# Kernel optimization log

Hardware: AMD Instinct MI355X
Metric: run time of the kernel (lower is better)

Reference implementation:

```python
import jax, jax.numpy as jnp
import numpy as np

N = 8192
C_IN = 512
C_INTER = 128  # in_channels // unit_nums = 512 // 4


def setup_inputs() -> dict:
    key = jax.random.key(0)
    ks = jax.random.split(key, 6)
    x = jax.random.normal(ks[0], (N, C_IN), dtype=jnp.float32)
    # Linear weights init: normal(0, 0.01); biases zero. Stored as [in, out].
    Wg = 0.01 * jax.random.normal(ks[1], (C_IN, C_INTER), dtype=jnp.float32)
    Wt = 0.01 * jax.random.normal(ks[2], (C_IN, C_INTER), dtype=jnp.float32)
    Wp = 0.01 * jax.random.normal(ks[3], (C_IN, C_INTER), dtype=jnp.float32)
    bg = jnp.zeros((C_INTER,), dtype=jnp.float32)
    bt = jnp.zeros((C_INTER,), dtype=jnp.float32)
    bp = jnp.zeros((C_INTER,), dtype=jnp.float32)
    # 1x1 conv weight (1, 2*C_INTER, 1, 1) flattened: first half hits theta, second half phi
    wcat = 0.01 * jax.random.normal(ks[4], (2 * C_INTER,), dtype=jnp.float32)
    return {"x": x, "Wg": Wg, "bg": bg, "Wt": Wt, "bt": bt, "Wp": Wp, "bp": bp, "wcat": wcat}


def reference(x, Wg, bg, Wt, bt, Wp, bp, wcat):
    n = x.shape[0]
    g_x = x @ Wg + bg          # [N, C_inter]
    theta = x @ Wt + bt        # [N, C_inter]
    phi = x @ Wp + bp          # [N, C_inter]
    c = theta.shape[1]
    # 1x1 conv over cat([theta_i, phi_j]) == w1.theta_i + w2.phi_j (outer sum), then ReLU
    a = theta @ wcat[:c]       # [N]
    b = phi @ wcat[c:]         # [N]
    f = jax.nn.relu(a[:, None] + b[None, :])  # [N, N]
    z = (f / n) @ g_x          # [N, C_inter]
    return z
```

## Files before the change

kernel.cpp:

```cpp
#include <hip/hip_runtime.h>

#define C_IN   512
#define C_INT  128
#define NBUCK  1024
#define NMAX   8192

typedef _Float16 half8 __attribute__((ext_vector_type(8)));
typedef short short8 __attribute__((ext_vector_type(8)));
typedef float floatx4 __attribute__((ext_vector_type(4)));


__device__ __forceinline__ int bucket_of(float v, float bmin, float inv_w) {
    float fk = (v - bmin) * inv_w;
    fk = fminf(fmaxf(fk, 0.f), (float)(NBUCK - 1));
    return (int)fk;
}

__device__ __forceinline__ short bf16rnd(float v) {
    unsigned u = __float_as_uint(v);
    return (short)((u + 0x7fffu + ((u >> 16) & 1u)) >> 16);
}


__global__ __launch_bounds__(256) void prep_kernel(
        const float* __restrict__ Wt, const float* __restrict__ Wp,
        const float* __restrict__ Wg, const float* __restrict__ wcat,
        const float* __restrict__ bt, const float* __restrict__ bp,
        float* __restrict__ ut, float* __restrict__ up, float* __restrict__ scal,
        unsigned short* __restrict__ WgT) {
    int t = threadIdx.x, bk = blockIdx.x;
    if (bk < 16) {
        const float* W  = (bk < 8) ? Wt : Wp;
        const float* wv = wcat + ((bk < 8) ? 0 : C_INT);
        float* dst      = (bk < 8) ? ut : up;
        int k = (bk & 7) * 64 + (t >> 2);
        int q = t & 3;
        const float4* row = (const float4*)(W + (size_t)k * C_INT);
        const float4* cv4 = (const float4*)wv;
        float s = 0.f;
        #pragma unroll
        for (int i = 0; i < 8; ++i) {
            float4 a = row[q * 8 + i];
            float4 c = cv4[q * 8 + i];
            s += a.x * c.x + a.y * c.y + a.z * c.z + a.w * c.w;
        }
        s += __shfl_xor(s, 1);
        s += __shfl_xor(s, 2);
        if (q == 0) dst[k] = s;
    } else if (bk == 16) {
        float sumsq = 0.f;
        const float4* w2v = (const float4*)(wcat + C_INT);
        for (int r = 0; r < 2; ++r) {
            int k = t * 2 + r;
            const float4* row = (const float4*)(Wp + (size_t)k * C_INT);
            float d = 0.f;
            #pragma unroll
            for (int i = 0; i < 32; ++i) {
                float4 a4 = row[i]; float4 c4 = w2v[i];
                d += a4.x * c4.x + a4.y * c4.y + a4.z * c4.z + a4.w * c4.w;
            }
            sumsq += d * d;
        }
        float s1p = (t < C_INT) ? bt[t] * wcat[t] : 0.f;
        float s2p = (t < C_INT) ? bp[t] * wcat[C_INT + t] : 0.f;
        for (int off = 32; off; off >>= 1) {
            s1p   += __shfl_down(s1p, off);
            s2p   += __shfl_down(s2p, off);
            sumsq += __shfl_down(sumsq, off);
        }
        __shared__ float red[12];
        int w = t >> 6, lane = t & 63;
        if (lane == 0) { red[w] = s1p; red[4 + w] = s2p; red[8 + w] = sumsq; }
        __syncthreads();
        if (t == 0) {
            float s0 = red[0] + red[1] + red[2] + red[3];
            float s1 = red[4] + red[5] + red[6] + red[7];
            float sq = red[8] + red[9] + red[10] + red[11];
            float sigma = sqrtf(sq);
            scal[0] = s0; scal[1] = s1;
            if (sigma > 1e-20f) {
                scal[2] = s1 - 8.f * sigma;
                scal[3] = (float)NBUCK / (16.f * sigma);
            } else {
                scal[2] = s1 - 1.f; scal[3] = 0.f;
            }
        }
    } else {
        __shared__ float tile[64][132];
        int kb = (bk - 17) * 64;
        #pragma unroll
        for (int it = 0; it < 8; ++it) {
            int idx = it * 256 + t;
            int r = idx >> 5, c4 = idx & 31;
            *(float4*)&tile[r][c4 * 4] =
                ((const float4*)(Wg + (size_t)(kb + r) * C_INT))[c4];
        }
        __syncthreads();
        int n = t & 127, kc = (t >> 7) * 32;
        unsigned pk[16];
        #pragma unroll
        for (int i = 0; i < 16; ++i) {
            unsigned lo = (unsigned short)bf16rnd(tile[kc + 2 * i][n]);
            unsigned hi = (unsigned short)bf16rnd(tile[kc + 2 * i + 1][n]);
            pk[i] = lo | (hi << 16);
        }
        uint4* dst = (uint4*)(WgT + (size_t)n * C_IN + kb + kc);
        #pragma unroll
        for (int i2 = 0; i2 < 4; ++i2) dst[i2] = *(uint4*)&pk[i2 * 4];
    }
}


__global__ __launch_bounds__(64) void gemm_mfma(
        const float* __restrict__ x, const unsigned short* __restrict__ WgT,
        const float* __restrict__ bg,
        const float* __restrict__ ut, const float* __restrict__ up,
        const float* __restrict__ scal,
        _Float16* __restrict__ g, float* __restrict__ a, float* __restrict__ b) {
    int lane = threadIdx.x;
    int i0 = blockIdx.x * 16;
    int m = lane & 15, q = lane >> 4;
    floatx4 accg[8] = {};
    floatx4 accab = {};
    const float* xrow = x + (size_t)(i0 + m) * C_IN + q * 8;
    const float* absrc = (m == 0) ? ut : up;
    #pragma unroll
    for (int ks = 0; ks < 16; ++ks) {
        int k0 = ks * 32;
        float4 f0 = *(const float4*)(xrow + k0);
        float4 f1 = *(const float4*)(xrow + k0 + 4);
        short8 af;
        af[0] = bf16rnd(f0.x); af[1] = bf16rnd(f0.y);
        af[2] = bf16rnd(f0.z); af[3] = bf16rnd(f0.w);
        af[4] = bf16rnd(f1.x); af[5] = bf16rnd(f1.y);
        af[6] = bf16rnd(f1.z); af[7] = bf16rnd(f1.w);
        short8 abf = {};
        if (m < 2) {
            float4 u0 = *(const float4*)(absrc + k0 + q * 8);
            float4 u1 = *(const float4*)(absrc + k0 + q * 8 + 4);
            abf[0] = bf16rnd(u0.x); abf[1] = bf16rnd(u0.y);
            abf[2] = bf16rnd(u0.z); abf[3] = bf16rnd(u0.w);
            abf[4] = bf16rnd(u1.x); abf[5] = bf16rnd(u1.y);
            abf[6] = bf16rnd(u1.z); abf[7] = bf16rnd(u1.w);
        }
        accab = __builtin_amdgcn_mfma_f32_16x16x32_bf16(af, abf, accab, 0, 0, 0);
        #pragma unroll
        for (int f = 0; f < 8; ++f) {
            short8 bfr = *(const short8*)(WgT + (size_t)(f * 16 + m) * C_IN + k0 + q * 8);
            accg[f] = __builtin_amdgcn_mfma_f32_16x16x32_bf16(af, bfr, accg[f], 0, 0, 0);
        }
    }
    #pragma unroll
    for (int f = 0; f < 8; ++f) {
        int col = f * 16 + m;
        float bgv = bg[col];
        #pragma unroll
        for (int r = 0; r < 4; ++r) {
            int row = i0 + q * 4 + r;
            g[(size_t)row * C_INT + col] = (_Float16)(accg[f][r] + bgv);
        }
    }
    if (m < 2) {
        float off = m ? scal[1] : scal[0];
        float* dst = m ? b : a;
        #pragma unroll
        for (int r = 0; r < 4; ++r) dst[i0 + q * 4 + r] = accab[r] + off;
    }
}


__global__ __launch_bounds__(1024) void bucketsuffix_kernel(
        const _Float16* __restrict__ g, const float* __restrict__ b,
        const float* __restrict__ scal,
        unsigned* __restrict__ offs_g, unsigned* __restrict__ list_g,
        float* __restrict__ P1, float* __restrict__ P2, int n) {
    __shared__ float bl[NMAX];
    __shared__ unsigned short ls[NMAX];
    __shared__ unsigned oh[NBUCK];
    __shared__ unsigned cur[NBUCK];
    __shared__ unsigned wtu[16];
    __shared__ float wt1[16], wt2[16];
    int t = threadIdx.x, c = blockIdx.x;
    int lane = t & 63, wv = t >> 6;
    float bmin = scal[2], inv_w = scal[3];
    ((float4*)bl)[t]        = ((const float4*)b)[t];
    ((float4*)bl)[1024 + t] = ((const float4*)b)[1024 + t];
    oh[t] = 0u; cur[t] = 0u;
    __syncthreads();
    int kb_[8];
    #pragma unroll
    for (int r = 0; r < 8; ++r) {
        kb_[r] = bucket_of(bl[t * 8 + r], bmin, inv_w);
        atomicAdd(&oh[kb_[r]], 1u);
    }
    __syncthreads();
    unsigned v = oh[t];
    #pragma unroll
    for (int d = 1; d < 64; d <<= 1) {
        unsigned u = __shfl_up(v, d);
        if (lane >= d) v += u;
    }
    if (lane == 63) wtu[wv] = v;
    __syncthreads();
    if (t < 16) {
        unsigned w = wtu[t];
        #pragma unroll
        for (int d = 1; d < 16; d <<= 1) {
            unsigned u = __shfl_up(w, d);
            if (t >= d) w += u;
        }
        wtu[t] = w;
    }
    __syncthreads();
    if (wv) v += wtu[wv - 1];
    oh[t] = v;
    __syncthreads();
    #pragma unroll
    for (int r = 0; r < 8; ++r) {
        int j = t * 8 + r;
        int k = kb_[r];
        unsigned e0 = k ? oh[k - 1] : 0u;
        unsigned pos = atomicAdd(&cur[k], 1u);
        ls[e0 + pos] = (unsigned short)j;
    }
    __syncthreads();
    if (c == 0) {
        #pragma unroll
        for (int r = 0; r < 8; ++r) list_g[r * 1024 + t] = (unsigned)ls[r * 1024 + t];
        offs_g[t + 1] = oh[t];
        if (t == 0) offs_g[0] = 0u;
    }
    unsigned e0 = t ? oh[t - 1] : 0u, e1 = oh[t];
    float h1 = 0.f, h2 = 0.f;
    for (unsigned e = e0; e < e1; ++e) {
        int j = ls[e];
        float bj = bl[j];
        float gv = (float)g[(size_t)j * C_INT + c];
        h1 += gv; h2 += bj * gv;
    }
    float v1 = h1, v2 = h2;
    #pragma unroll
    for (int d = 1; d < 64; d <<= 1) {
        float u1 = __shfl_up(v1, d), u2 = __shfl_up(v2, d);
        if (lane >= d) { v1 += u1; v2 += u2; }
    }
    if (lane == 63) { wt1[wv] = v1; wt2[wv] = v2; }
    __syncthreads();
    if (t < 16) {
        float w1 = wt1[t], w2 = wt2[t];
        #pragma unroll
        for (int d = 1; d < 16; d <<= 1) {
            float u1 = __shfl_up(w1, d), u2 = __shfl_up(w2, d);
            if (t >= d) { w1 += u1; w2 += u2; }
        }
        wt1[t] = w1; wt2[t] = w2;
    }
    __syncthreads();
    if (wv) { v1 += wt1[wv - 1]; v2 += wt2[wv - 1]; }
    float tot1 = wt1[15], tot2 = wt2[15];
    P1[(size_t)t * C_INT + c] = tot1 - v1 + h1;
    P2[(size_t)t * C_INT + c] = tot2 - v2 + h2;
    if (t == 0) {
        P1[(size_t)NBUCK * C_INT + c] = 0.f;
        P2[(size_t)NBUCK * C_INT + c] = 0.f;
    }
}


__global__ __launch_bounds__(128) void out_kernel(
        const float* __restrict__ a, const float* __restrict__ b,
        const _Float16* __restrict__ g, const float* __restrict__ scal,
        const unsigned* __restrict__ offs, const unsigned* __restrict__ list,
        const float* __restrict__ P1, const float* __restrict__ P2,
        float* __restrict__ out, int n, float inv_n) {
    int i = blockIdx.x, c = threadIdx.x;
    float ai = a[i], thr = -ai;
    float bmin = scal[2], inv_w = scal[3];
    int ki = bucket_of(thr, bmin, inv_w);
    size_t base = (size_t)(ki + 1) * C_INT;
    float acc = ai * P1[base + c] + P2[base + c];
    unsigned e0 = offs[ki], e1 = offs[ki + 1];
    for (unsigned e = e0; e < e1; ++e) {
        unsigned j = list[e];
        float bj = b[j];
        if (bj > thr) acc += (ai + bj) * (float)g[(size_t)j * C_INT + c];
    }
    out[(size_t)i * C_INT + c] = acc * inv_n;
}


extern "C" void kernel_launch(void* const* d_in, const int* in_sizes, int n_in,
                              void* d_out, int out_size, void* d_ws, size_t ws_size,
                              hipStream_t stream) {
    const float* x    = (const float*)d_in[0];
    const float* Wg   = (const float*)d_in[1];
    const float* bg   = (const float*)d_in[2];
    const float* Wt   = (const float*)d_in[3];
    const float* bt   = (const float*)d_in[4];
    const float* Wp   = (const float*)d_in[5];
    const float* bp   = (const float*)d_in[6];
    const float* wcat = (const float*)d_in[7];
    float* out = (float*)d_out;
    int n = in_sizes[0] / C_IN;

    char* w = (char*)d_ws;
    size_t off = 0;
    auto alloc = [&](size_t bytes) -> void* {
        void* p = w + off;
        off += (bytes + 255) & ~(size_t)255;
        return p;
    };
    float*          ut   = (float*)alloc(C_IN * 4);
    float*          up   = (float*)alloc(C_IN * 4);
    float*          scal = (float*)alloc(16);
    float*          a    = (float*)alloc((size_t)n * 4);
    float*          b    = (float*)alloc((size_t)n * 4);
    unsigned*       offs = (unsigned*)alloc((NBUCK + 1) * 4);
    unsigned*       list = (unsigned*)alloc((size_t)n * 4);
    _Float16*       g    = (_Float16*)alloc((size_t)n * C_INT * 2);
    unsigned short* WgT  = (unsigned short*)alloc((size_t)C_INT * C_IN * 2);
    float*          P1   = (float*)alloc((size_t)(NBUCK + 1) * C_INT * 4);
    float*          P2   = (float*)alloc((size_t)(NBUCK + 1) * C_INT * 4);

    prep_kernel<<<25, 256, 0, stream>>>(Wt, Wp, Wg, wcat, bt, bp, ut, up, scal, WgT);
    gemm_mfma<<<n / 16, 64, 0, stream>>>(x, WgT, bg, ut, up, scal, g, a, b);
    bucketsuffix_kernel<<<C_INT, 1024, 0, stream>>>(g, b, scal, offs, list, P1, P2, n);
    out_kernel<<<n, C_INT, 0, stream>>>(a, b, g, scal, offs, list, P1, P2,
                                        out, n, 1.0f / (float)n);
}
```

Measured before the change: 161.0 us.

## Replace per-channel bucket kernel with single sort plus segmented per-element suffix sums

Raises the bucket count to 8192 and sorts b once in a single block, using packed 16-bit histogram counters, instead of re-sorting in each of 128 channel blocks. It then builds full per-element suffix sums of g and b*g through a two-level segmented scan (segment sums, then expansion), so out_kernel only scans a tiny residual bucket, staged through shared memory. The intent is to shrink both the redundant sort work and the per-row residual loop. In exchange it adds two extra launches and writes large Pr1/Pr2 arrays of (n+1)x128 floats. The expand kernel also sums later segments serially, which is quadratic across segments.

```diff
diff --git a/kernel.cpp b/kernel.cpp
--- a/kernel.cpp
+++ b/kernel.cpp
@@ -2,10 +2,10 @@
 
 #define C_IN   512
 #define C_INT  128
-#define NBUCK  1024
-#define NMAX   8192
-
-typedef _Float16 half8 __attribute__((ext_vector_type(8)));
+#define NBUCK  8192
+#define SEG    32
+#define NSEG   256
+
 typedef short short8 __attribute__((ext_vector_type(8)));
 typedef float floatx4 __attribute__((ext_vector_type(4)));
 
@@ -169,32 +169,37 @@
 }
 
 
-__global__ __launch_bounds__(1024) void bucketsuffix_kernel(
-        const _Float16* __restrict__ g, const float* __restrict__ b,
-        const float* __restrict__ scal,
-        unsigned* __restrict__ offs_g, unsigned* __restrict__ list_g,
-        float* __restrict__ P1, float* __restrict__ P2, int n) {
-    __shared__ float bl[NMAX];
-    __shared__ unsigned short ls[NMAX];
-    __shared__ unsigned oh[NBUCK];
-    __shared__ unsigned cur[NBUCK];
+__global__ __launch_bounds__(1024) void sort_kernel(
+        const float* __restrict__ b, const float* __restrict__ scal,
+        unsigned* __restrict__ offs_g, unsigned short* __restrict__ perm_g,
+        float* __restrict__ bsort_g) {
+    __shared__ unsigned oh[NBUCK / 2];
+    __shared__ unsigned cur[NBUCK / 2];
+    __shared__ unsigned short ls[8192];
     __shared__ unsigned wtu[16];
-    __shared__ float wt1[16], wt2[16];
-    int t = threadIdx.x, c = blockIdx.x;
-    int lane = t & 63, wv = t >> 6;
+    int t = threadIdx.x, lane = t & 63, wv = t >> 6;
+    #pragma unroll
+    for (int r = 0; r < 4; ++r) { oh[t + r * 1024] = 0u; cur[t + r * 1024] = 0u; }
+    __syncthreads();
     float bmin = scal[2], inv_w = scal[3];
-    ((float4*)bl)[t]        = ((const float4*)b)[t];
-    ((float4*)bl)[1024 + t] = ((const float4*)b)[1024 + t];
-    oh[t] = 0u; cur[t] = 0u;
-    __syncthreads();
-    int kb_[8];
+    int kb[8];
+    float bv[8];
     #pragma unroll
     for (int r = 0; r < 8; ++r) {
-        kb_[r] = bucket_of(bl[t * 8 + r], bmin, inv_w);
-        atomicAdd(&oh[kb_[r]], 1u);
-    }
-    __syncthreads();
-    unsigned v = oh[t];
+        int j = t + r * 1024;
+        bv[r] = b[j];
+        kb[r] = bucket_of(bv[r], bmin, inv_w);
+        atomicAdd(&oh[kb[r] >> 1], (kb[r] & 1) ? 0x10000u : 1u);
+    }
+    __syncthreads();
+    unsigned h[8], p = 0;
+    #pragma unroll
+    for (int w = 0; w < 4; ++w) {
+        unsigned word = oh[t * 4 + w];
+        p += word & 0xffffu;  h[w * 2]     = p;
+        p += word >> 16;      h[w * 2 + 1] = p;
+    }
+    unsigned v = p;
     #pragma unroll
     for (int d = 1; d < 64; d <<= 1) {
         unsigned u = __shfl_up(v, d);
@@ -212,78 +217,115 @@
         wtu[t] = w;
     }
     __syncthreads();
-    if (wv) v += wtu[wv - 1];
-    oh[t] = v;
+    unsigned base = (v - p) + (wv ? wtu[wv - 1] : 0u);
+    #pragma unroll
+    for (int w = 0; w < 4; ++w) {
+        unsigned lo = base + h[w * 2], hi = base + h[w * 2 + 1];
+        oh[t * 4 + w] = lo | (hi << 16);
+        offs_g[t * 8 + w * 2 + 1] = lo;
+        offs_g[t * 8 + w * 2 + 2] = hi;
+    }
+    if (t == 0) offs_g[0] = 0u;
     __syncthreads();
     #pragma unroll
     for (int r = 0; r < 8; ++r) {
-        int j = t * 8 + r;
-        int k = kb_[r];
-        unsigned e0 = k ? oh[k - 1] : 0u;
-        unsigned pos = atomicAdd(&cur[k], 1u);
-        ls[e0 + pos] = (unsigned short)j;
-    }
-    __syncthreads();
-    if (c == 0) {
-        #pragma unroll
-        for (int r = 0; r < 8; ++r) list_g[r * 1024 + t] = (unsigned)ls[r * 1024 + t];
-        offs_g[t + 1] = oh[t];
-        if (t == 0) offs_g[0] = 0u;
-    }
-    unsigned e0 = t ? oh[t - 1] : 0u, e1 = oh[t];
-    float h1 = 0.f, h2 = 0.f;
-    for (unsigned e = e0; e < e1; ++e) {
+        int j = t + r * 1024;
+        int k = kb[r];
+        unsigned st = 0u;
+        if (k > 0) {
+            unsigned word = oh[(k - 1) >> 1];
+            st = ((k - 1) & 1) ? (word >> 16) : (word & 0xffffu);
+        }
+        unsigned old = atomicAdd(&cur[k >> 1], (k & 1) ? 0x10000u : 1u);
+        unsigned pos = (k & 1) ? (old >> 16) : (old & 0xffffu);
+        ls[st + pos] = (unsigned short)j;
+    }
+    __syncthreads();
+    #pragma unroll
+    for (int r = 0; r < 8; ++r) {
+        int e = t + r * 1024;
         int j = ls[e];
-        float bj = bl[j];
-        float gv = (float)g[(size_t)j * C_INT + c];
-        h1 += gv; h2 += bj * gv;
-    }
-    float v1 = h1, v2 = h2;
-    #pragma unroll
-    for (int d = 1; d < 64; d <<= 1) {
-        float u1 = __shfl_up(v1, d), u2 = __shfl_up(v2, d);
-        if (lane >= d) { v1 += u1; v2 += u2; }
-    }
-    if (lane == 63) { wt1[wv] = v1; wt2[wv] = v2; }
-    __syncthreads();
-    if (t < 16) {
-        float w1 = wt1[t], w2 = wt2[t];
-        #pragma unroll
-        for (int d = 1; d < 16; d <<= 1) {
-            float u1 = __shfl_up(w1, d), u2 = __shfl_up(w2, d);
-            if (t >= d) { w1 += u1; w2 += u2; }
-        }
-        wt1[t] = w1; wt2[t] = w2;
-    }
-    __syncthreads();
-    if (wv) { v1 += wt1[wv - 1]; v2 += wt2[wv - 1]; }
-    float tot1 = wt1[15], tot2 = wt2[15];
-    P1[(size_t)t * C_INT + c] = tot1 - v1 + h1;
-    P2[(size_t)t * C_INT + c] = tot2 - v2 + h2;
-    if (t == 0) {
-        P1[(size_t)NBUCK * C_INT + c] = 0.f;
-        P2[(size_t)NBUCK * C_INT + c] = 0.f;
+        perm_g[e] = (unsigned short)j;
+        bsort_g[e] = b[j];
+    }
+}
+
+
+__global__ __launch_bounds__(128) void segsum_kernel(
+        const _Float16* __restrict__ g, const unsigned short* __restrict__ perm,
+        const float* __restrict__ bsort,
+        float* __restrict__ seg1, float* __restrict__ seg2) {
+    __shared__ int pj[SEG];
+    __shared__ float pb[SEG];
+    int s = blockIdx.x, t = threadIdx.x;
+    if (t < SEG) { pj[t] = perm[s * SEG + t]; pb[t] = bsort[s * SEG + t]; }
+    __syncthreads();
+    float a1 = 0.f, a2 = 0.f;
+    #pragma unroll
+    for (int e = 0; e < SEG; ++e) {
+        float gv = (float)g[(size_t)pj[e] * C_INT + t];
+        a1 += gv; a2 += pb[e] * gv;
+    }
+    seg1[s * C_INT + t] = a1;
+    seg2[s * C_INT + t] = a2;
+}
+
+
+__global__ __launch_bounds__(128) void expand_kernel(
+        const _Float16* __restrict__ g, const unsigned short* __restrict__ perm,
+        const float* __restrict__ bsort,
+        const float* __restrict__ seg1, const float* __restrict__ seg2,
+        float* __restrict__ Pr1, float* __restrict__ Pr2) {
+    __shared__ int pj[SEG];
+    __shared__ float pb[SEG];
+    int s = blockIdx.x, t = threadIdx.x;
+    if (t < SEG) { pj[t] = perm[s * SEG + t]; pb[t] = bsort[s * SEG + t]; }
+    __syncthreads();
+    float r1 = 0.f, r2 = 0.f;
+    for (int s2 = s + 1; s2 < NSEG; ++s2) {
+        r1 += seg1[s2 * C_INT + t];
+        r2 += seg2[s2 * C_INT + t];
+    }
+    #pragma unroll
+    for (int e = SEG - 1; e >= 0; --e) {
+        float gv = (float)g[(size_t)pj[e] * C_INT + t];
+        r1 += gv; r2 += pb[e] * gv;
+        size_t idx = (size_t)(s * SEG + e) * C_INT + t;
+        Pr1[idx] = r1; Pr2[idx] = r2;
+    }
+    if (s == NSEG - 1) {
+        Pr1[(size_t)8192 * C_INT + t] = 0.f;
+        Pr2[(size_t)8192 * C_INT + t] = 0.f;
     }
 }
 
 
 __global__ __launch_bounds__(128) void out_kernel(
-        const float* __restrict__ a, const float* __restrict__ b,
-        const _Float16* __restrict__ g, const float* __restrict__ scal,
-        const unsigned* __restrict__ offs, const unsigned* __restrict__ list,
-        const float* __restrict__ P1, const float* __restrict__ P2,
-        float* __restrict__ out, int n, float inv_n) {
+        const float* __restrict__ a, const float* __restrict__ scal,
+        const _Float16* __restrict__ g,
+        const unsigned* __restrict__ offs, const unsigned short* __restrict__ perm,
+        const float* __restrict__ bsort,
+        const float* __restrict__ Pr1, const float* __restrict__ Pr2,
+        float* __restrict__ out, float inv_n) {
+    __shared__ int pj[128];
+    __shared__ float pb[128];
     int i = blockIdx.x, c = threadIdx.x;
     float ai = a[i], thr = -ai;
     float bmin = scal[2], inv_w = scal[3];
     int ki = bucket_of(thr, bmin, inv_w);
-    size_t base = (size_t)(ki + 1) * C_INT;
-    float acc = ai * P1[base + c] + P2[base + c];
     unsigned e0 = offs[ki], e1 = offs[ki + 1];
-    for (unsigned e = e0; e < e1; ++e) {
-        unsigned j = list[e];
-        float bj = b[j];
-        if (bj > thr) acc += (ai + bj) * (float)g[(size_t)j * C_INT + c];
+    size_t base = (size_t)e1 * C_INT + c;
+    float acc = ai * Pr1[base] + Pr2[base];
+    for (unsigned be = e0; be < e1; be += 128) {
+        unsigned cnt = min(128u, e1 - be);
+        if ((unsigned)c < cnt) { pj[c] = perm[be + c]; pb[c] = bsort[be + c]; }
+        __syncthreads();
+        for (unsigned r = 0; r < cnt; ++r) {
+            float bj = pb[r];
+            if (bj > thr)
+                acc += (ai + bj) * (float)g[(size_t)pj[r] * C_INT + c];
+        }
+        __syncthreads();
     }
     out[(size_t)i * C_INT + c] = acc * inv_n;
 }
@@ -310,21 +352,26 @@
         off += (bytes + 255) & ~(size_t)255;
         return p;
     };
-    float*          ut   = (float*)alloc(C_IN * 4);
-    float*          up   = (float*)alloc(C_IN * 4);
-    float*          scal = (float*)alloc(16);
-    float*          a    = (float*)alloc((size_t)n * 4);
-    float*          b    = (float*)alloc((size_t)n * 4);
-    unsigned*       offs = (unsigned*)alloc((NBUCK + 1) * 4);
-    unsigned*       list = (unsigned*)alloc((size_t)n * 4);
-    _Float16*       g    = (_Float16*)alloc((size_t)n * C_INT * 2);
-    unsigned short* WgT  = (unsigned short*)alloc((size_t)C_INT * C_IN * 2);
-    float*          P1   = (float*)alloc((size_t)(NBUCK + 1) * C_INT * 4);
-    float*          P2   = (float*)alloc((size_t)(NBUCK + 1) * C_INT * 4);
+    float*          ut    = (float*)alloc(C_IN * 4);
+    float*          up    = (float*)alloc(C_IN * 4);
+    float*          scal  = (float*)alloc(16);
+    float*          a     = (float*)alloc((size_t)n * 4);
+    float*          b     = (float*)alloc((size_t)n * 4);
+    unsigned*       offs  = (unsigned*)alloc((size_t)(NBUCK + 1) * 4);
+    unsigned short* perm  = (unsigned short*)alloc((size_t)n * 2);
+    float*          bsort = (float*)alloc((size_t)n * 4);
+    _Float16*       g     = (_Float16*)alloc((size_t)n * C_INT * 2);
+    unsigned short* WgT   = (unsigned short*)alloc((size_t)C_INT * C_IN * 2);
+    float*          seg1  = (float*)alloc((size_t)NSEG * C_INT * 4);
+    float*          seg2  = (float*)alloc((size_t)NSEG * C_INT * 4);
+    float*          Pr1   = (float*)alloc((size_t)(n + 1) * C_INT * 4);
+    float*          Pr2   = (float*)alloc((size_t)(n + 1) * C_INT * 4);
 
     prep_kernel<<<25, 256, 0, stream>>>(Wt, Wp, Wg, wcat, bt, bp, ut, up, scal, WgT);
     gemm_mfma<<<n / 16, 64, 0, stream>>>(x, WgT, bg, ut, up, scal, g, a, b);
-    bucketsuffix_kernel<<<C_INT, 1024, 0, stream>>>(g, b, scal, offs, list, P1, P2, n);
-    out_kernel<<<n, C_INT, 0, stream>>>(a, b, g, scal, offs, list, P1, P2,
-                                        out, n, 1.0f / (float)n);
-}
+    sort_kernel<<<1, 1024, 0, stream>>>(b, scal, offs, perm, bsort);
+    segsum_kernel<<<NSEG, 128, 0, stream>>>(g, perm, bsort, seg1, seg2);
+    expand_kernel<<<NSEG, 128, 0, stream>>>(g, perm, bsort, seg1, seg2, Pr1, Pr2);
+    out_kernel<<<n, 128, 0, stream>>>(a, scal, g, offs, perm, bsort, Pr1, Pr2,
+                                      out, 1.0f / (float)n);
+}
```

After: 160.4 us. About the same (-0.4%).

## Fuse bucket-suffix and output kernels into one per-channel kernel; split-K GEMM across four waves

Applied to the files above, without the earlier changes.

The GEMM now uses four waves per block. Each wave handles a quarter of the K dimension, and the partial accumulators are reduced through shared memory. This raises parallelism per output tile. The separate bucket-suffix and per-row output kernels become a single post_kernel with one block per channel. That block keeps the bucketed list, the sorted b values and the suffix sums P1/P2 in LDS and computes every output row for its channel, removing the global P1/P2/list round trips and one launch. In exchange only 128 blocks do all the output work, and each writes output with stride 128 floats (uncoalesced), so parallelism and store efficiency may suffer.

```diff
diff --git a/kernel.cpp b/kernel.cpp
--- a/kernel.cpp
+++ b/kernel.cpp
@@ -3,9 +3,7 @@
 #define C_IN   512
 #define C_INT  128
 #define NBUCK  1024
-#define NMAX   8192
-
-typedef _Float16 half8 __attribute__((ext_vector_type(8)));
+
 typedef short short8 __attribute__((ext_vector_type(8)));
 typedef float floatx4 __attribute__((ext_vector_type(4)));
 
@@ -111,13 +109,17 @@
 }
 
 
-__global__ __launch_bounds__(64) void gemm_mfma(
+#define RSTR 66
+
+__global__ __launch_bounds__(256) void gemm_mfma(
         const float* __restrict__ x, const unsigned short* __restrict__ WgT,
         const float* __restrict__ bg,
         const float* __restrict__ ut, const float* __restrict__ up,
         const float* __restrict__ scal,
         _Float16* __restrict__ g, float* __restrict__ a, float* __restrict__ b) {
-    int lane = threadIdx.x;
+    __shared__ float red[3][36][RSTR];
+    int tid = threadIdx.x;
+    int lane = tid & 63, wv = tid >> 6;
     int i0 = blockIdx.x * 16;
     int m = lane & 15, q = lane >> 4;
     floatx4 accg[8] = {};
@@ -125,8 +127,8 @@
     const float* xrow = x + (size_t)(i0 + m) * C_IN + q * 8;
     const float* absrc = (m == 0) ? ut : up;
     #pragma unroll
-    for (int ks = 0; ks < 16; ++ks) {
-        int k0 = ks * 32;
+    for (int ks = 0; ks < 4; ++ks) {
+        int k0 = (wv * 4 + ks) * 32;
         float4 f0 = *(const float4*)(xrow + k0);
         float4 f1 = *(const float4*)(xrow + k0 + 4);
         short8 af;
@@ -150,50 +152,82 @@
             accg[f] = __builtin_amdgcn_mfma_f32_16x16x32_bf16(af, bfr, accg[f], 0, 0, 0);
         }
     }
-    #pragma unroll
-    for (int f = 0; f < 8; ++f) {
-        int col = f * 16 + m;
-        float bgv = bg[col];
-        #pragma unroll
-        for (int r = 0; r < 4; ++r) {
-            int row = i0 + q * 4 + r;
-            g[(size_t)row * C_INT + col] = (_Float16)(accg[f][r] + bgv);
-        }
-    }
-    if (m < 2) {
-        float off = m ? scal[1] : scal[0];
-        float* dst = m ? b : a;
-        #pragma unroll
-        for (int r = 0; r < 4; ++r) dst[i0 + q * 4 + r] = accab[r] + off;
-    }
-}
-
-
-__global__ __launch_bounds__(1024) void bucketsuffix_kernel(
-        const _Float16* __restrict__ g, const float* __restrict__ b,
-        const float* __restrict__ scal,
-        unsigned* __restrict__ offs_g, unsigned* __restrict__ list_g,
-        float* __restrict__ P1, float* __restrict__ P2, int n) {
-    __shared__ float bl[NMAX];
-    __shared__ unsigned short ls[NMAX];
-    __shared__ unsigned oh[NBUCK];
-    __shared__ unsigned cur[NBUCK];
-    __shared__ unsigned wtu[16];
-    __shared__ float wt1[16], wt2[16];
+    if (wv) {
+        #pragma unroll
+        for (int f = 0; f < 8; ++f)
+            #pragma unroll
+            for (int r = 0; r < 4; ++r)
+                red[wv - 1][f * 4 + r][lane] = accg[f][r];
+        #pragma unroll
+        for (int r = 0; r < 4; ++r)
+            red[wv - 1][32 + r][lane] = accab[r];
+    }
+    __syncthreads();
+    if (wv == 0) {
+        #pragma unroll
+        for (int w = 0; w < 3; ++w) {
+            #pragma unroll
+            for (int f = 0; f < 8; ++f)
+                #pragma unroll
+                for (int r = 0; r < 4; ++r)
+                    accg[f][r] += red[w][f * 4 + r][lane];
+            #pragma unroll
+            for (int r = 0; r < 4; ++r)
+                accab[r] += red[w][32 + r][lane];
+        }
+        #pragma unroll
+        for (int f = 0; f < 8; ++f) {
+            int col = f * 16 + m;
+            float bgv = bg[col];
+            #pragma unroll
+            for (int r = 0; r < 4; ++r) {
+                int row = i0 + q * 4 + r;
+                g[(size_t)row * C_INT + col] = (_Float16)(accg[f][r] + bgv);
+            }
+        }
+        if (m < 2) {
+            float off = m ? scal[1] : scal[0];
+            float* dst = m ? b : a;
+            #pragma unroll
+            for (int r = 0; r < 4; ++r) dst[i0 + q * 4 + r] = accab[r] + off;
+        }
+    }
+}
+
+
+__global__ __launch_bounds__(1024, 4) void post_kernel(
+        const _Float16* __restrict__ g, const float* __restrict__ a,
+        const float* __restrict__ b, const float* __restrict__ scal,
+        float* __restrict__ out, float inv_n) {
+    __shared__ __align__(16) unsigned char smem[65536];
+    float*          bs  = (float*)smem;
+    unsigned short* ls  = (unsigned short*)(smem + 32768);
+    unsigned*       oh  = (unsigned*)(smem + 49152);
+    unsigned*       cur = (unsigned*)(smem + 53248);
+    float*          P1  = (float*)(smem + 57344);
+    float*          P2  = (float*)(smem + 61440);
+    unsigned* wtu = (unsigned*)(smem + 57344);
+    float*    wt1 = (float*)(smem + 53248);
+    float*    wt2 = (float*)(smem + 53248 + 64);
+
     int t = threadIdx.x, c = blockIdx.x;
     int lane = t & 63, wv = t >> 6;
     float bmin = scal[2], inv_w = scal[3];
-    ((float4*)bl)[t]        = ((const float4*)b)[t];
-    ((float4*)bl)[1024 + t] = ((const float4*)b)[1024 + t];
+
     oh[t] = 0u; cur[t] = 0u;
     __syncthreads();
-    int kb_[8];
+
+    int kb[8];
+    float bv[8];
     #pragma unroll
     for (int r = 0; r < 8; ++r) {
-        kb_[r] = bucket_of(bl[t * 8 + r], bmin, inv_w);
-        atomicAdd(&oh[kb_[r]], 1u);
-    }
-    __syncthreads();
+        int j = t + r * 1024;
+        bv[r] = b[j];
+        kb[r] = bucket_of(bv[r], bmin, inv_w);
+        atomicAdd(&oh[kb[r]], 1u);
+    }
+    __syncthreads();
+
     unsigned v = oh[t];
     #pragma unroll
     for (int d = 1; d < 64; d <<= 1) {
@@ -215,28 +249,24 @@
     if (wv) v += wtu[wv - 1];
     oh[t] = v;
     __syncthreads();
+
     #pragma unroll
     for (int r = 0; r < 8; ++r) {
-        int j = t * 8 + r;
-        int k = kb_[r];
-        unsigned e0 = k ? oh[k - 1] : 0u;
+        int j = t + r * 1024;
+        int k = kb[r];
+        unsigned st = k ? oh[k - 1] : 0u;
         unsigned pos = atomicAdd(&cur[k], 1u);
-        ls[e0 + pos] = (unsigned short)j;
-    }
-    __syncthreads();
-    if (c == 0) {
-        #pragma unroll
-        for (int r = 0; r < 8; ++r) list_g[r * 1024 + t] = (unsigned)ls[r * 1024 + t];
-        offs_g[t + 1] = oh[t];
-        if (t == 0) offs_g[0] = 0u;
-    }
+        ls[st + pos] = (unsigned short)j;
+        bs[st + pos] = bv[r];
+    }
+    __syncthreads();
+
     unsigned e0 = t ? oh[t - 1] : 0u, e1 = oh[t];
     float h1 = 0.f, h2 = 0.f;
     for (unsigned e = e0; e < e1; ++e) {
         int j = ls[e];
-        float bj = bl[j];
         float gv = (float)g[(size_t)j * C_INT + c];
-        h1 += gv; h2 += bj * gv;
+        h1 += gv; h2 += bs[e] * gv;
     }
     float v1 = h1, v2 = h2;
     #pragma unroll
@@ -258,34 +288,25 @@
     __syncthreads();
     if (wv) { v1 += wt1[wv - 1]; v2 += wt2[wv - 1]; }
     float tot1 = wt1[15], tot2 = wt2[15];
-    P1[(size_t)t * C_INT + c] = tot1 - v1 + h1;
-    P2[(size_t)t * C_INT + c] = tot2 - v2 + h2;
-    if (t == 0) {
-        P1[(size_t)NBUCK * C_INT + c] = 0.f;
-        P2[(size_t)NBUCK * C_INT + c] = 0.f;
-    }
-}
-
-
-__global__ __launch_bounds__(128) void out_kernel(
-        const float* __restrict__ a, const float* __restrict__ b,
-        const _Float16* __restrict__ g, const float* __restrict__ scal,
-        const unsigned* __restrict__ offs, const unsigned* __restrict__ list,
-        const float* __restrict__ P1, const float* __restrict__ P2,
-        float* __restrict__ out, int n, float inv_n) {
-    int i = blockIdx.x, c = threadIdx.x;
-    float ai = a[i], thr = -ai;
-    float bmin = scal[2], inv_w = scal[3];
-    int ki = bucket_of(thr, bmin, inv_w);
-    size_t base = (size_t)(ki + 1) * C_INT;
-    float acc = ai * P1[base + c] + P2[base + c];
-    unsigned e0 = offs[ki], e1 = offs[ki + 1];
-    for (unsigned e = e0; e < e1; ++e) {
-        unsigned j = list[e];
-        float bj = b[j];
-        if (bj > thr) acc += (ai + bj) * (float)g[(size_t)j * C_INT + c];
-    }
-    out[(size_t)i * C_INT + c] = acc * inv_n;
+    __syncthreads();
+    P1[t] = tot1 - v1 + h1;
+    P2[t] = tot2 - v2 + h2;
+    __syncthreads();
+
+    #pragma unroll
+    for (int r = 0; r < 8; ++r) {
+        int i = t + r * 1024;
+        float ai = a[i], thr = -ai;
+        int ki = bucket_of(thr, bmin, inv_w);
+        float acc = (ki + 1 < NBUCK) ? (ai * P1[ki + 1] + P2[ki + 1]) : 0.f;
+        unsigned f0 = ki ? oh[ki - 1] : 0u, f1 = oh[ki];
+        for (unsigned e = f0; e < f1; ++e) {
+            float bj = bs[e];
+            if (bj > thr)
+                acc += (ai + bj) * (float)g[(size_t)ls[e] * C_INT + c];
+        }
+        out[(size_t)i * C_INT + c] = acc * inv_n;
+    }
 }
 
 
@@ -315,16 +336,10 @@
     float*          scal = (float*)alloc(16);
     float*          a    = (float*)alloc((size_t)n * 4);
     float*          b    = (float*)alloc((size_t)n * 4);
-    unsigned*       offs = (unsigned*)alloc((NBUCK + 1) * 4);
-    unsigned*       list = (unsigned*)alloc((size_t)n * 4);
     _Float16*       g    = (_Float16*)alloc((size_t)n * C_INT * 2);
     unsigned short* WgT  = (unsigned short*)alloc((size_t)C_INT * C_IN * 2);
-    float*          P1   = (float*)alloc((size_t)(NBUCK + 1) * C_INT * 4);
-    float*          P2   = (float*)alloc((size_t)(NBUCK + 1) * C_INT * 4);
 
     prep_kernel<<<25, 256, 0, stream>>>(Wt, Wp, Wg, wcat, bt, bp, ut, up, scal, WgT);
-    gemm_mfma<<<n / 16, 64, 0, stream>>>(x, WgT, bg, ut, up, scal, g, a, b);
-    bucketsuffix_kernel<<<C_INT, 1024, 0, stream>>>(g, b, scal, offs, list, P1, P2, n);
-    out_kernel<<<n, C_INT, 0, stream>>>(a, b, g, scal, offs, list, P1, P2,
-                                        out, n, 1.0f / (float)n);
-}
+    gemm_mfma<<<n / 16, 256, 0, stream>>>(x, WgT, bg, ut, up, scal, g, a, b);
+    post_kernel<<<C_INT, 1024, 0, stream>>>(g, a, b, scal, out, 1.0f / (float)n);
+}
```

Result: slower. 245.1 us (+52.3%).
